# Kernel tuning notes

Hardware: AMD Instinct MI355X
Metric: run time of the kernel (lower is better)

Reference implementation:

```python
import jax, jax.numpy as jnp
import numpy as np

DIM_H = 384
EPS = 0.5
HID = 768
NN = 3   # num_normal_labels (B,I,O)
NL = 7   # num_labels (O, B/I x POS/NEG/NEU)


def _make_w_trans():
    # ote_vocab: B=0, I=1, O=2 ; ts_vocab: O=0, B-POS=1, B-NEG=2, B-NEU=3, I-POS=4, I-NEG=5, I-NEU=6
    W = np.zeros((NN, NL), dtype=np.float32)
    W[0, 1] = W[0, 2] = W[0, 3] = 1.0 / 3.0  # B -> B-*
    W[1, 4] = W[1, 5] = W[1, 6] = 1.0 / 3.0  # I -> I-*
    W[2, 0] = 1.0                            # O -> O
    return jnp.asarray(W)


def setup_inputs() -> dict:
    key = jax.random.key(0)
    ks = jax.random.split(key, 16)
    B, S = 32, 512
    s = 0.02
    inp = {
        'x': jax.random.normal(ks[0], (B, S, HID), jnp.float32),
        'attention_mask': jnp.ones((B, S), jnp.int32),
        'labels': jax.random.randint(ks[1], (B, S), 0, NL, jnp.int32),
        'labels_normal': jax.random.randint(ks[2], (B, S), 0, NN, jnp.int32),
        'W_fc_normal': jax.random.normal(ks[3], (HID, NN), jnp.float32) * s,
        'b_fc_normal': jnp.zeros((NN,), jnp.float32),
        'w_ih_f': jax.random.normal(ks[4], (4 * DIM_H, HID), jnp.float32) * s,
        'w_hh_f': jax.random.normal(ks[5], (4 * DIM_H, DIM_H), jnp.float32) * s,
        'b_f': jnp.zeros((4 * DIM_H,), jnp.float32),
        'w_ih_b': jax.random.normal(ks[6], (4 * DIM_H, HID), jnp.float32) * s,
        'w_hh_b': jax.random.normal(ks[7], (4 * DIM_H, DIM_H), jnp.float32) * s,
        'b_b': jnp.zeros((4 * DIM_H,), jnp.float32),
        'W_gate': jax.random.uniform(ks[8], (2 * DIM_H, 2 * DIM_H), jnp.float32, -0.2, 0.2),
        'W_fc_upper': jax.random.normal(ks[9], (2 * DIM_H, NL), jnp.float32) * s,
        'b_fc_upper': jnp.zeros((NL,), jnp.float32),
        'W_trans': _make_w_trans(),
    }
    return inp


def _lstm_dir(xs, w_ih, w_hh, b):
    # xs: [S, B, HID] time-major; PyTorch gate order i,f,g,o
    B = xs.shape[1]
    pre = jnp.einsum('sbh,gh->sbg', xs, w_ih) + b  # precompute input projections

    def step(carry, p_t):
        h, c = carry
        g = p_t + h @ w_hh.T
        i, f, gg, o = jnp.split(g, 4, axis=-1)
        c = jax.nn.sigmoid(f) * c + jax.nn.sigmoid(i) * jnp.tanh(gg)
        h = jax.nn.sigmoid(o) * jnp.tanh(c)
        return (h, c), h

    init = (jnp.zeros((B, DIM_H), xs.dtype), jnp.zeros((B, DIM_H), xs.dtype))
    _, hs = jax.lax.scan(step, init, pre)
    return hs  # [S, B, DIM_H]


def _masked_ce(logits, labels, mask):
    logp = jax.nn.log_softmax(logits, axis=-1)
    nll = -jnp.take_along_axis(logp, labels[..., None].astype(jnp.int32), axis=-1)[..., 0]
    m = mask.astype(logits.dtype)
    return jnp.sum(nll * m) / jnp.sum(m)


def reference(x, attention_mask, labels, labels_normal, W_fc_normal, b_fc_normal,
              w_ih_f, w_hh_f, b_f, w_ih_b, w_hh_b, b_b, W_gate,
              W_fc_upper, b_fc_upper, W_trans):
    z_t = x @ W_fc_normal + b_fc_normal                      # [B,S,NN]
    loss = _masked_ce(z_t, labels_normal, attention_mask)

    xs = jnp.transpose(x, (1, 0, 2))                         # [S,B,HID]
    hf = _lstm_dir(xs, w_ih_f, w_hh_f, b_f)
    hb = _lstm_dir(xs[::-1], w_ih_b, w_hh_b, b_b)[::-1]
    h_s = jnp.concatenate([hf, hb], axis=-1)                 # [S,B,2*DIM_H]

    # gated highway recurrence: gates depend only on h_s -> batched matmul + linear scan
    g = jax.nn.sigmoid(h_s @ W_gate)                         # [S,B,768]

    def gate_step(h_prev, inp):
        ht, gt = inp
        h = gt * ht + (1.0 - gt) * h_prev
        return h, h

    _, rest = jax.lax.scan(gate_step, h_s[0], (h_s[1:], g[1:]))
    h_tilde = jnp.concatenate([h_s[:1], rest], axis=0)       # [S,B,768]
    h_tilde = jnp.transpose(h_tilde, (1, 0, 2))              # [B,S,768]; dropout = identity (eval)

    z_s = h_tilde @ W_fc_upper + b_fc_upper                  # [B,S,NL]
    p = jax.nn.softmax(z_t, axis=-1)
    alpha = EPS * jnp.sum(p * p, axis=-1, keepdims=True)     # [B,S,1]
    z_s_prime = z_t @ W_trans                                # [B,S,NL]
    z_s_tilde = z_s_prime * alpha + z_s * (1.0 - alpha)

    loss = loss + _masked_ce(z_s_tilde, labels, attention_mask)
    return loss, z_s_tilde
```

## Files before the change

kernel.cpp:

```cpp
#include <hip/hip_runtime.h>

#define B_SZ   32
#define S_LEN  512
#define HID    768
#define DH     384
#define G4     1536
#define NPOS   16384
#define EPS_C  0.5f
#define NCH    24576
#define CHK    64
#define NCHK   8

typedef _Float16 h2 __attribute__((ext_vector_type(2)));
typedef short bf16x8 __attribute__((ext_vector_type(8)));
typedef float f32x4 __attribute__((ext_vector_type(4)));

static __device__ __forceinline__ float sigm(float x) { return 1.0f / (1.0f + __expf(-x)); }
static __device__ __forceinline__ float tanh_fast(float x) {
    return 1.0f - 2.0f / (__expf(2.0f * x) + 1.0f);
}

static __device__ __forceinline__ unsigned short f2bf(float f) {
    union { float f; unsigned u; } v; v.f = f;
    unsigned r = v.u + 0x7FFF + ((v.u >> 16) & 1);
    return (unsigned short)(r >> 16);
}
static __device__ __forceinline__ float bf2f(unsigned short u) {
    union { unsigned u; float f; } v; v.u = ((unsigned)u) << 16; return v.f;
}

static __device__ __forceinline__ float wred(float v) {
#pragma unroll
    for (int off = 32; off > 0; off >>= 1) v += __shfl_down(v, off, 64);
    return v;
}

static __device__ __forceinline__ float dot2acc(h2 a, h2 b, float c) {
#if __has_builtin(__builtin_amdgcn_fdot2)
    return __builtin_amdgcn_fdot2(a, b, c, false);
#else
    return c + (float)a.x * (float)b.x + (float)a.y * (float)b.y;
#endif
}

__global__ void wprep(const float* __restrict__ wf, const float* __restrict__ wb,
                      unsigned* __restrict__ wpk) {
    int gid = blockIdx.x * 256 + threadIdx.x;
    int d = (gid >= 294912) ? 1 : 0;
    int j = gid - d * 294912;
    const float* src = d ? wb : wf;
    _Float16 a = (_Float16)src[2 * j];
    _Float16 b = (_Float16)src[2 * j + 1];
    unsigned pa = __builtin_bit_cast(unsigned short, a);
    unsigned pb = __builtin_bit_cast(unsigned short, b);
    wpk[(size_t)d * 294912 + j] = pa | (pb << 16);
}

__global__ __launch_bounds__(256) void cast_bf16(
    const float* __restrict__ src, unsigned short* __restrict__ dst, int n4) {
    int i = blockIdx.x * 256 + threadIdx.x;
    if (i >= n4) return;
    float4 v = *(const float4*)(src + (size_t)i * 4);
    ushort4 o;
    o.x = f2bf(v.x); o.y = f2bf(v.y); o.z = f2bf(v.z); o.w = f2bf(v.w);
    *(ushort4*)(dst + (size_t)i * 4) = o;
}

__global__ __launch_bounds__(256) void wgt_prep(
    const float* __restrict__ Wg, unsigned short* __restrict__ Wgt) {
    int i = blockIdx.x * 256 + threadIdx.x;
    int k = i / 768, n = i - k * 768;
    Wgt[(size_t)n * 768 + k] = f2bf(Wg[i]);
}

__global__ __launch_bounds__(256) void zt_kernel(
    const float* __restrict__ x, const int* __restrict__ amask,
    const int* __restrict__ labn, const float* __restrict__ Wfc,
    const float* __restrict__ bfc, const float* __restrict__ Wtr,
    float* __restrict__ alpha, float* __restrict__ zsp,
    float* __restrict__ p0, float* __restrict__ p2) {
    const int gid  = blockIdx.x * blockDim.x + threadIdx.x;
    const int pos  = gid >> 6, lane = gid & 63, wv = threadIdx.x >> 6;
    __shared__ float r0[4], r2[4];
    const float* xp = x + (size_t)pos * HID;
    float a0 = 0.f, a1 = 0.f, a2 = 0.f;
#pragma unroll
    for (int j = 0; j < 12; ++j) {
        int k = lane + (j << 6);
        float xv = xp[k];
        a0 += xv * Wfc[k * 3 + 0];
        a1 += xv * Wfc[k * 3 + 1];
        a2 += xv * Wfc[k * 3 + 2];
    }
    a0 = wred(a0); a1 = wred(a1); a2 = wred(a2);
    if (lane == 0) {
        float z0 = a0 + bfc[0], z1 = a1 + bfc[1], z2 = a2 + bfc[2];
        float mx = fmaxf(z0, fmaxf(z1, z2));
        float e0 = __expf(z0 - mx), e1 = __expf(z1 - mx), e2 = __expf(z2 - mx);
        float se = e0 + e1 + e2;
        float m  = (float)amask[pos];
        int  lab = labn[pos];
        float zl = (lab == 0) ? z0 : ((lab == 1) ? z1 : z2);
        r0[wv] = (mx + __logf(se) - zl) * m;
        r2[wv] = m;
        float q0 = e0 / se, q1 = e1 / se, q2 = e2 / se;
        alpha[pos] = EPS_C * (q0 * q0 + q1 * q1 + q2 * q2);
#pragma unroll
        for (int cc = 0; cc < 7; ++cc)
            zsp[(size_t)pos * 7 + cc] = z0 * Wtr[cc] + z1 * Wtr[7 + cc] + z2 * Wtr[14 + cc];
    }
    __syncthreads();
    if (threadIdx.x == 0) {
        p0[blockIdx.x] = r0[0] + r0[1] + r0[2] + r0[3];
        p2[blockIdx.x] = r2[0] + r2[1] + r2[2] + r2[3];
    }
}

__global__ __launch_bounds__(256) void gemm_mfma(
    const unsigned short* __restrict__ A, const unsigned short* __restrict__ B,
    const float* __restrict__ bias, void* __restrict__ Cout,
    int M, int N, int K, int mode) {
    __shared__ __align__(16) unsigned short As[128][40];
    __shared__ __align__(16) unsigned short Bs[128][40];
    const int tid = threadIdx.x;
    const int m0 = blockIdx.y * 128, n0 = blockIdx.x * 128;
    const int wave = tid >> 6, lane = tid & 63;
    const int wm = (wave & 1) * 64, wn = (wave >> 1) * 64;
    const int lm = lane & 15, quad = lane >> 4;
    f32x4 acc[4][4] = {};

    for (int k0 = 0; k0 < K; k0 += 32) {
#pragma unroll
        for (int r = 0; r < 2; ++r) {
            int seg = tid + r * 256;
            int row = seg >> 2, c16 = (seg & 3) << 3;
            uint4 va = *(const uint4*)(A + (size_t)(m0 + row) * K + k0 + c16);
            *(uint4*)&As[row][c16] = va;
            uint4 vb = *(const uint4*)(B + (size_t)(n0 + row) * K + k0 + c16);
            *(uint4*)&Bs[row][c16] = vb;
        }
        __syncthreads();
        bf16x8 af[4], bfr[4];
#pragma unroll
        for (int i = 0; i < 4; ++i) {
            af[i]  = *(const bf16x8*)&As[wm + i * 16 + lm][quad * 8];
            bfr[i] = *(const bf16x8*)&Bs[wn + i * 16 + lm][quad * 8];
        }
#pragma unroll
        for (int mi = 0; mi < 4; ++mi)
#pragma unroll
            for (int ni = 0; ni < 4; ++ni)
                acc[mi][ni] = __builtin_amdgcn_mfma_f32_16x16x32_bf16(
                    af[mi], bfr[ni], acc[mi][ni], 0, 0, 0);
        __syncthreads();
    }

    const int rbase = quad * 4;
#pragma unroll
    for (int mi = 0; mi < 4; ++mi) {
#pragma unroll
        for (int ni = 0; ni < 4; ++ni) {
            const int col = n0 + wn + ni * 16 + lm;
            const float bv = (mode == 0) ? bias[col] : 0.0f;
#pragma unroll
            for (int r = 0; r < 4; ++r) {
                const int row = m0 + wm + mi * 16 + rbase + r;
                float v = acc[mi][ni][r];
                if (mode == 0)
                    ((unsigned short*)Cout)[(size_t)row * N + col] = f2bf(v + bv);
                else
                    ((unsigned short*)Cout)[(size_t)row * N + col] = f2bf(sigm(v));
            }
        }
    }
}

#define WLOAD(i) const uint4 wr##i = wq[i];
#define WDOT(i) \
    a0 = dot2acc(__builtin_bit_cast(h2, wr##i.x), hp[4*(i)+0], a0); \
    a1 = dot2acc(__builtin_bit_cast(h2, wr##i.y), hp[4*(i)+1], a1); \
    a2 = dot2acc(__builtin_bit_cast(h2, wr##i.z), hp[4*(i)+2], a2); \
    a3 = dot2acc(__builtin_bit_cast(h2, wr##i.w), hp[4*(i)+3], a3);

__global__ __launch_bounds__(768) void lstm_scan5(
    const unsigned* __restrict__ wpk,
    const unsigned short* __restrict__ pre,
    unsigned short* __restrict__ h_sb,
    unsigned long long* __restrict__ hx64) {
    const int blk   = blockIdx.x;
    const int chain = blk & 63;
    const int bp    = blk >> 6;
    const int d = chain >> 5, b = chain & 31;
    const int tid = threadIdx.x;
    const int r = tid >> 1, p = tid & 1;
    const int g = r / 96;
    const int u = r - g * 96;
    const int base = bp * 96;
    const int G = g * 384 + base + u;

    __shared__ __align__(16) _Float16 lh16[2][384];
    __shared__ float    lpreV[384];
    __shared__ unsigned lpreT[384];

    const uint4* wq = (const uint4*)(wpk + ((size_t)d * 1536 + G) * 192 + p * 96);
    WLOAD(0)  WLOAD(1)  WLOAD(2)  WLOAD(3)  WLOAD(4)  WLOAD(5)
    WLOAD(6)  WLOAD(7)  WLOAD(8)  WLOAD(9)  WLOAD(10) WLOAD(11)
    WLOAD(12) WLOAD(13) WLOAD(14) WLOAD(15) WLOAD(16) WLOAD(17)
    WLOAD(18) WLOAD(19) WLOAD(20) WLOAD(21) WLOAD(22) WLOAD(23)

    const unsigned short* prb = pre + ((size_t)d * B_SZ + b) * S_LEN * G4;
    float c = 0.0f;

    for (int s = 0; s < S_LEN; ++s) {
        const int t = d ? (S_LEN - 1 - s) : s;
        const int lb = s & 1;
        float prev = bf2f(prb[(size_t)t * G4 + G]);

        if (s == 0) {
            if (tid < 384) { lh16[0][tid] = (_Float16)0.0f; lpreT[tid] = 0xFFFFFFFFu; }
        } else if (tid < 288) {
            const int uu = tid + (tid >= base ? 96 : 0);
            const unsigned long long* srcp =
                hx64 + ((size_t)((s - 1) & 1) * 64 + chain) * 384 + uu;
            unsigned long long v =
                __hip_atomic_load(srcp, __ATOMIC_RELAXED, __HIP_MEMORY_SCOPE_AGENT);
            while ((unsigned)(v >> 32) != (unsigned)(s - 1)) {
                __builtin_amdgcn_s_sleep(1);
                v = __hip_atomic_load(srcp, __ATOMIC_RELAXED, __HIP_MEMORY_SCOPE_AGENT);
            }
            lh16[lb][uu] = (_Float16)__builtin_bit_cast(float, (unsigned)v);
        }
        __syncthreads();

        {
            const h2* hp = ((const h2*)lh16[lb]) + p * 96;
            float a0 = (p == 0) ? prev : 0.0f, a1 = 0.f, a2 = 0.f, a3 = 0.f;
            WDOT(0)  WDOT(1)  WDOT(2)  WDOT(3)  WDOT(4)  WDOT(5)
            WDOT(6)  WDOT(7)  WDOT(8)  WDOT(9)  WDOT(10) WDOT(11)
            WDOT(12) WDOT(13) WDOT(14) WDOT(15) WDOT(16) WDOT(17)
            WDOT(18) WDOT(19) WDOT(20) WDOT(21) WDOT(22) WDOT(23)
            float acc = (a0 + a1) + (a2 + a3);
            float full = acc + __shfl_xor(acc, 1, 64);
            if (p == 0) {
                lpreV[r] = full;
                __hip_atomic_store(&lpreT[r], (unsigned)s, __ATOMIC_RELEASE,
                                   __HIP_MEMORY_SCOPE_WORKGROUP);
            }
        }

        if (tid < 96) {
            const unsigned sv = (unsigned)s;
#pragma unroll
            for (int j = 0; j < 4; ++j) {
                unsigned* tp = &lpreT[j * 96 + tid];
                while (__hip_atomic_load(tp, __ATOMIC_ACQUIRE,
                                         __HIP_MEMORY_SCOPE_WORKGROUP) != sv) {}
            }
            float gi = lpreV[tid], gf = lpreV[96 + tid];
            float gg = lpreV[192 + tid], go = lpreV[288 + tid];
            c = sigm(gf) * c + sigm(gi) * tanh_fast(gg);
            float h = sigm(go) * tanh_fast(c);
            unsigned long long v = ((unsigned long long)sv << 32)
                                 | (unsigned long long)__builtin_bit_cast(unsigned, h);
            __hip_atomic_store(hx64 + ((size_t)lb * 64 + chain) * 384 + base + tid,
                               v, __ATOMIC_RELAXED, __HIP_MEMORY_SCOPE_AGENT);
            h_sb[((size_t)t * B_SZ + b) * HID + d * DH + base + tid] = f2bf(h);
            lh16[lb ^ 1][base + tid] = (_Float16)h;
        }
    }
}

__global__ __launch_bounds__(256) void gscanA(
    const unsigned short* __restrict__ g, const unsigned short* __restrict__ hsb,
    float2* __restrict__ ab) {
    int id = blockIdx.x * 256 + threadIdx.x;
    int chunk = id / NCH, chain = id - chunk * NCH;
    int t0 = chunk * CHK;
    float A = 1.f, Bv = 0.f;
    for (int i = 0; i < CHK; ++i) {
        int t = t0 + i;
        size_t idx = (size_t)t * NCH + chain;
        float gv = bf2f(g[idx]);
        float hv = bf2f(hsb[idx]);
        float a = (t == 0) ? 0.f : (1.f - gv);
        float bb = (t == 0) ? hv : gv * hv;
        A  = a * A;
        Bv = a * Bv + bb;
    }
    ab[id] = make_float2(A, Bv);
}

__global__ __launch_bounds__(256) void gscanB(
    const float2* __restrict__ ab, float* __restrict__ cin) {
    int chain = blockIdx.x * 256 + threadIdx.x;
    float h = 0.f;
#pragma unroll
    for (int j = 0; j < NCHK; ++j) {
        cin[(size_t)j * NCH + chain] = h;
        float2 t = ab[(size_t)j * NCH + chain];
        h = t.x * h + t.y;
    }
}

__global__ __launch_bounds__(256) void gscanC(
    const unsigned short* __restrict__ g, unsigned short* __restrict__ hsb,
    const float* __restrict__ cin) {
    int id = blockIdx.x * 256 + threadIdx.x;
    int chunk = id / NCH, chain = id - chunk * NCH;
    int t0 = chunk * CHK;
    float h = cin[(size_t)chunk * NCH + chain];
    for (int i = 0; i < CHK; ++i) {
        int t = t0 + i;
        size_t idx = (size_t)t * NCH + chain;
        float gv = bf2f(g[idx]);
        float v  = bf2f(hsb[idx]);
        h = (t == 0) ? v : (gv * v + (1.f - gv) * h);
        hsb[idx] = f2bf(h);
    }
}

__global__ __launch_bounds__(256) void final_k(
    const unsigned short* __restrict__ ht, const float* __restrict__ Wup,
    const float* __restrict__ bup, const float* __restrict__ alpha,
    const float* __restrict__ zsp, const int* __restrict__ labels,
    const int* __restrict__ amask, float* __restrict__ out, float* __restrict__ p1) {
    const int gid = blockIdx.x * blockDim.x + threadIdx.x;
    const int pos = gid >> 6, lane = gid & 63, wv = threadIdx.x >> 6;
    __shared__ float r1[4];
    const int bb = pos >> 9, tt = pos & 511;
    const unsigned short* hp = ht + (size_t)tt * (B_SZ * HID) + (size_t)bb * HID;
    float acc[7] = {};
#pragma unroll
    for (int j = 0; j < 12; ++j) {
        int k = lane + (j << 6);
        float hv = bf2f(hp[k]);
        const float* wr = Wup + k * 7;
#pragma unroll
        for (int cc = 0; cc < 7; ++cc) acc[cc] += hv * wr[cc];
    }
#pragma unroll
    for (int cc = 0; cc < 7; ++cc) acc[cc] = wred(acc[cc]);
    if (lane == 0) {
        float al = alpha[pos];
        float z[7], mx = -1e30f;
#pragma unroll
        for (int cc = 0; cc < 7; ++cc) {
            float v = acc[cc] + bup[cc];
            v = zsp[(size_t)pos * 7 + cc] * al + v * (1.0f - al);
            z[cc] = v;
            mx = fmaxf(mx, v);
            out[1 + (size_t)pos * 7 + cc] = v;
        }
        float se = 0.f;
#pragma unroll
        for (int cc = 0; cc < 7; ++cc) se += __expf(z[cc] - mx);
        float lse = mx + __logf(se);
        int lab = labels[pos];
        float zl = z[0];
#pragma unroll
        for (int cc = 1; cc < 7; ++cc) if (lab == cc) zl = z[cc];
        float m = (float)amask[pos];
        r1[wv] = (lse - zl) * m;
    }
    __syncthreads();
    if (threadIdx.x == 0)
        p1[blockIdx.x] = r1[0] + r1[1] + r1[2] + r1[3];
}

__global__ __launch_bounds__(256) void loss_k(
    const float* __restrict__ p0, const float* __restrict__ p1,
    const float* __restrict__ p2, float* __restrict__ out) {
    const int tid = threadIdx.x, lane = tid & 63, wv = tid >> 6;
    __shared__ float rs[4][3];
    float s0 = 0.f, s1 = 0.f, s2 = 0.f;
    for (int i = tid; i < 4096; i += 256) {
        s0 += p0[i]; s1 += p1[i]; s2 += p2[i];
    }
    s0 = wred(s0); s1 = wred(s1); s2 = wred(s2);
    if (lane == 0) { rs[wv][0] = s0; rs[wv][1] = s1; rs[wv][2] = s2; }
    __syncthreads();
    if (tid == 0) {
        float t0 = rs[0][0] + rs[1][0] + rs[2][0] + rs[3][0];
        float t1 = rs[0][1] + rs[1][1] + rs[2][1] + rs[3][1];
        float t2 = rs[0][2] + rs[1][2] + rs[2][2] + rs[3][2];
        out[0] = t0 / t2 + t1 / t2;
    }
}

extern "C" void kernel_launch(void* const* d_in, const int* in_sizes, int n_in,
                              void* d_out, int out_size, void* d_ws, size_t ws_size,
                              hipStream_t stream) {
    const float* x     = (const float*)d_in[0];
    const int*   amask = (const int*)d_in[1];
    const int*   labels= (const int*)d_in[2];
    const int*   labn  = (const int*)d_in[3];
    const float* Wfc   = (const float*)d_in[4];
    const float* bfc   = (const float*)d_in[5];
    const float* wihf  = (const float*)d_in[6];
    const float* whhf  = (const float*)d_in[7];
    const float* bf    = (const float*)d_in[8];
    const float* wihb  = (const float*)d_in[9];
    const float* whhb  = (const float*)d_in[10];
    const float* bb    = (const float*)d_in[11];
    const float* Wg    = (const float*)d_in[12];
    const float* Wup   = (const float*)d_in[13];
    const float* bup   = (const float*)d_in[14];
    const float* Wtr   = (const float*)d_in[15];
    float* out = (float*)d_out;
    (void)in_sizes; (void)n_in; (void)out_size; (void)ws_size;

    char* ws = (char*)d_ws;
    size_t off = 0;
    auto alloc = [&](size_t bytes) -> char* {
        char* p = ws + off;
        off = (off + bytes + 255) & ~(size_t)255;
        return p;
    };
    unsigned* w16buf    = (unsigned*)alloc((size_t)2 * 1536 * 192 * 4);
    unsigned short* pre = (unsigned short*)alloc((size_t)2 * NPOS * G4 * 2);
    unsigned short* xb  = (unsigned short*)alloc((size_t)NPOS * HID * 2);
    unsigned short* wfb = (unsigned short*)alloc((size_t)G4 * HID * 2);
    unsigned short* wbb = (unsigned short*)alloc((size_t)G4 * HID * 2);
    unsigned short* wgt = (unsigned short*)alloc((size_t)HID * HID * 2);
    float* alpha        = (float*)alloc((size_t)NPOS * 4);
    float* zsp          = (float*)alloc((size_t)NPOS * 7 * 4);
    unsigned long long* hx64 = (unsigned long long*)alloc((size_t)2 * 64 * 384 * 8);
    float2* ab          = (float2*)alloc((size_t)NCHK * NCH * 8);
    float* cin          = (float*)alloc((size_t)NCHK * NCH * 4);
    float* part0        = (float*)alloc(4096 * 4);
    float* part1        = (float*)alloc(4096 * 4);
    float* part2        = (float*)alloc(4096 * 4);
    unsigned short* gbuf = (unsigned short*)pre;
    unsigned short* h_sb = xb;


    wprep<<<2304, 256, 0, stream>>>(whhf, whhb, w16buf);
    cast_bf16<<<12288, 256, 0, stream>>>(x, xb, NPOS * HID / 4);
    cast_bf16<<<1152, 256, 0, stream>>>(wihf, wfb, G4 * HID / 4);
    cast_bf16<<<1152, 256, 0, stream>>>(wihb, wbb, G4 * HID / 4);
    wgt_prep<<<2304, 256, 0, stream>>>(Wg, wgt);

    zt_kernel<<<4096, 256, 0, stream>>>(x, amask, labn, Wfc, bfc, Wtr, alpha, zsp,
                                        part0, part2);

    gemm_mfma<<<dim3(12, 128), 256, 0, stream>>>(xb, wfb, bf, pre, NPOS, G4, HID, 0);
    gemm_mfma<<<dim3(12, 128), 256, 0, stream>>>(xb, wbb, bb, pre + (size_t)NPOS * G4,
                                                 NPOS, G4, HID, 0);

    lstm_scan5<<<256, 768, 0, stream>>>(w16buf, pre, h_sb, hx64);

    gemm_mfma<<<dim3(6, 128), 256, 0, stream>>>(h_sb, wgt, nullptr, gbuf, NPOS, HID, HID, 1);

    gscanA<<<768, 256, 0, stream>>>(gbuf, h_sb, ab);
    gscanB<<<96, 256, 0, stream>>>(ab, cin);
    gscanC<<<768, 256, 0, stream>>>(gbuf, h_sb, cin);

    final_k<<<4096, 256, 0, stream>>>(h_sb, Wup, bup, alpha, zsp, labels, amask, out, part1);

    loss_k<<<1, 256, 0, stream>>>(part0, part1, part2, out);
}
```

Before: 1.270 ms.

## Repartition LSTM scan so each block handles four chains over a row slice

```diff
diff --git a/kernel.cpp b/kernel.cpp
--- a/kernel.cpp
+++ b/kernel.cpp
@@ -175,97 +175,138 @@
     }
 }
 
-#define WLOAD(i) const uint4 wr##i = wq[i];
-#define WDOT(i) \
-    a0 = dot2acc(__builtin_bit_cast(h2, wr##i.x), hp[4*(i)+0], a0); \
-    a1 = dot2acc(__builtin_bit_cast(h2, wr##i.y), hp[4*(i)+1], a1); \
-    a2 = dot2acc(__builtin_bit_cast(h2, wr##i.z), hp[4*(i)+2], a2); \
-    a3 = dot2acc(__builtin_bit_cast(h2, wr##i.w), hp[4*(i)+3], a3);
-
-__global__ __launch_bounds__(768) void lstm_scan5(
+#define D16(W, X, A, Bx) { const uint4 xx = (X); \
+    A  = dot2acc(__builtin_bit_cast(h2, W.x), __builtin_bit_cast(h2, xx.x), A); \
+    Bx = dot2acc(__builtin_bit_cast(h2, W.y), __builtin_bit_cast(h2, xx.y), Bx); \
+    A  = dot2acc(__builtin_bit_cast(h2, W.z), __builtin_bit_cast(h2, xx.z), A); \
+    Bx = dot2acc(__builtin_bit_cast(h2, W.w), __builtin_bit_cast(h2, xx.w), Bx); }
+
+__global__ __launch_bounds__(768)
+__attribute__((amdgpu_waves_per_eu(3, 3)))
+void lstm_scan6(
     const unsigned* __restrict__ wpk,
     const unsigned short* __restrict__ pre,
     unsigned short* __restrict__ h_sb,
     unsigned long long* __restrict__ hx64) {
-    const int blk   = blockIdx.x;
-    const int chain = blk & 63;
-    const int bp    = blk >> 6;
-    const int d = chain >> 5, b = chain & 31;
+    const int blk = blockIdx.x;
+    const int grp = blk & 15;
+    const int rp  = blk >> 4;
+    const int d   = grp >> 3;
     const int tid = threadIdx.x;
-    const int r = tid >> 1, p = tid & 1;
-    const int g = r / 96;
-    const int u = r - g * 96;
-    const int base = bp * 96;
-    const int G = g * 384 + base + u;
-
-    __shared__ __align__(16) _Float16 lh16[2][384];
+    const int r   = tid >> 3;
+    const int p   = tid & 7;
+    const int g   = r / 24;
+    const int u   = r - g * 24;
+    const int G   = g * 384 + rp * 24 + u;
+
+    __shared__ __align__(16) _Float16 lh16[2][4][384];
     __shared__ float    lpreV[384];
     __shared__ unsigned lpreT[384];
 
-    const uint4* wq = (const uint4*)(wpk + ((size_t)d * 1536 + G) * 192 + p * 96);
-    WLOAD(0)  WLOAD(1)  WLOAD(2)  WLOAD(3)  WLOAD(4)  WLOAD(5)
-    WLOAD(6)  WLOAD(7)  WLOAD(8)  WLOAD(9)  WLOAD(10) WLOAD(11)
-    WLOAD(12) WLOAD(13) WLOAD(14) WLOAD(15) WLOAD(16) WLOAD(17)
-    WLOAD(18) WLOAD(19) WLOAD(20) WLOAD(21) WLOAD(22) WLOAD(23)
-
-    const unsigned short* prb = pre + ((size_t)d * B_SZ + b) * S_LEN * G4;
+    const uint4* wq = (const uint4*)wpk + (size_t)(d * 1536 + G) * 48 + p * 6;
+    const uint4 w0 = wq[0], w1 = wq[1], w2 = wq[2],
+                w3 = wq[3], w4 = wq[4], w5 = wq[5];
+
+    const int chp = grp * 4 + (p & 3);
+    const unsigned short* prb =
+        pre + ((size_t)d * B_SZ + (chp & 31)) * S_LEN * G4 + G;
+
     float c = 0.0f;
 
     for (int s = 0; s < S_LEN; ++s) {
-        const int t = d ? (S_LEN - 1 - s) : s;
+        const int t  = d ? (S_LEN - 1 - s) : s;
         const int lb = s & 1;
-        float prev = bf2f(prb[(size_t)t * G4 + G]);
+        float prev = 0.0f;
+        if (p < 4) prev = bf2f(prb[(size_t)t * G4]);
 
         if (s == 0) {
-            if (tid < 384) { lh16[0][tid] = (_Float16)0.0f; lpreT[tid] = 0xFFFFFFFFu; }
-        } else if (tid < 288) {
-            const int uu = tid + (tid >= base ? 96 : 0);
-            const unsigned long long* srcp =
-                hx64 + ((size_t)((s - 1) & 1) * 64 + chain) * 384 + uu;
-            unsigned long long v =
-                __hip_atomic_load(srcp, __ATOMIC_RELAXED, __HIP_MEMORY_SCOPE_AGENT);
-            while ((unsigned)(v >> 32) != (unsigned)(s - 1)) {
-                __builtin_amdgcn_s_sleep(1);
-                v = __hip_atomic_load(srcp, __ATOMIC_RELAXED, __HIP_MEMORY_SCOPE_AGENT);
+            if (tid < 384) lpreT[tid] = 0xFFFFFFFFu;
+            const int cia = (tid >= 384) ? 1 : 0;
+            const int j = tid - cia * 384;
+            lh16[0][cia][j]     = (_Float16)0.0f;
+            lh16[0][cia + 2][j] = (_Float16)0.0f;
+        } else {
+            const int cia = (tid >= 384) ? 1 : 0;
+            const int j = tid - cia * 384;
+            if ((unsigned)(j - rp * 24) >= 24u) {
+                const unsigned long long* sp0 =
+                    hx64 + ((size_t)((s - 1) & 1) * 64 + grp * 4 + cia) * 384 + j;
+                const unsigned want = (unsigned)(s - 1);
+                unsigned long long v0 =
+                    __hip_atomic_load(sp0, __ATOMIC_RELAXED, __HIP_MEMORY_SCOPE_AGENT);
+                unsigned long long v1 =
+                    __hip_atomic_load(sp0 + 768, __ATOMIC_RELAXED, __HIP_MEMORY_SCOPE_AGENT);
+                while ((unsigned)(v0 >> 32) != want) {
+                    __builtin_amdgcn_s_sleep(1);
+                    v0 = __hip_atomic_load(sp0, __ATOMIC_RELAXED, __HIP_MEMORY_SCOPE_AGENT);
+                }
+                while ((unsigned)(v1 >> 32) != want) {
+                    __builtin_amdgcn_s_sleep(1);
+                    v1 = __hip_atomic_load(sp0 + 768, __ATOMIC_RELAXED, __HIP_MEMORY_SCOPE_AGENT);
+                }
+                lh16[lb][cia][j]     = (_Float16)__builtin_bit_cast(float, (unsigned)v0);
+                lh16[lb][cia + 2][j] = (_Float16)__builtin_bit_cast(float, (unsigned)v1);
             }
-            lh16[lb][uu] = (_Float16)__builtin_bit_cast(float, (unsigned)v);
         }
         __syncthreads();
 
         {
-            const h2* hp = ((const h2*)lh16[lb]) + p * 96;
-            float a0 = (p == 0) ? prev : 0.0f, a1 = 0.f, a2 = 0.f, a3 = 0.f;
-            WDOT(0)  WDOT(1)  WDOT(2)  WDOT(3)  WDOT(4)  WDOT(5)
-            WDOT(6)  WDOT(7)  WDOT(8)  WDOT(9)  WDOT(10) WDOT(11)
-            WDOT(12) WDOT(13) WDOT(14) WDOT(15) WDOT(16) WDOT(17)
-            WDOT(18) WDOT(19) WDOT(20) WDOT(21) WDOT(22) WDOT(23)
-            float acc = (a0 + a1) + (a2 + a3);
-            float full = acc + __shfl_xor(acc, 1, 64);
-            if (p == 0) {
-                lpreV[r] = full;
-                __hip_atomic_store(&lpreT[r], (unsigned)s, __ATOMIC_RELEASE,
+            const char* hb = (const char*)&lh16[lb][0][0] + p * 96;
+            const uint4* h0 = (const uint4*)(hb);
+            const uint4* h1 = (const uint4*)(hb + 768);
+            const uint4* h2q = (const uint4*)(hb + 1536);
+            const uint4* h3 = (const uint4*)(hb + 2304);
+            float a0 = 0.f, a1 = 0.f, a2 = 0.f, a3 = 0.f;
+            float b0 = 0.f, b1 = 0.f, b2 = 0.f, b3 = 0.f;
+            if      (p == 0) a0 = prev;
+            else if (p == 1) a1 = prev;
+            else if (p == 2) a2 = prev;
+            else if (p == 3) a3 = prev;
+            D16(w0, h0[0], a0, b0) D16(w1, h0[1], a0, b0) D16(w2, h0[2], a0, b0)
+            D16(w3, h0[3], a0, b0) D16(w4, h0[4], a0, b0) D16(w5, h0[5], a0, b0)
+            D16(w0, h1[0], a1, b1) D16(w1, h1[1], a1, b1) D16(w2, h1[2], a1, b1)
+            D16(w3, h1[3], a1, b1) D16(w4, h1[4], a1, b1) D16(w5, h1[5], a1, b1)
+            D16(w0, h2q[0], a2, b2) D16(w1, h2q[1], a2, b2) D16(w2, h2q[2], a2, b2)
+            D16(w3, h2q[3], a2, b2) D16(w4, h2q[4], a2, b2) D16(w5, h2q[5], a2, b2)
+            D16(w0, h3[0], a3, b3) D16(w1, h3[1], a3, b3) D16(w2, h3[2], a3, b3)
+            D16(w3, h3[3], a3, b3) D16(w4, h3[4], a3, b3) D16(w5, h3[5], a3, b3)
+            a0 += b0; a1 += b1; a2 += b2; a3 += b3;
+#pragma unroll
+            for (int off = 1; off < 8; off <<= 1) {
+                a0 += __shfl_xor(a0, off, 64);
+                a1 += __shfl_xor(a1, off, 64);
+                a2 += __shfl_xor(a2, off, 64);
+                a3 += __shfl_xor(a3, off, 64);
+            }
+            if (p < 4) {
+                float av = (p == 0) ? a0 : (p == 1) ? a1 : (p == 2) ? a2 : a3;
+                lpreV[p * 96 + r] = av;
+                __hip_atomic_store(&lpreT[p * 96 + r], (unsigned)s, __ATOMIC_RELEASE,
                                    __HIP_MEMORY_SCOPE_WORKGROUP);
             }
         }
 
         if (tid < 96) {
+            const int ci = tid / 24, uu = tid - ci * 24;
             const unsigned sv = (unsigned)s;
-#pragma unroll
-            for (int j = 0; j < 4; ++j) {
-                unsigned* tp = &lpreT[j * 96 + tid];
-                while (__hip_atomic_load(tp, __ATOMIC_ACQUIRE,
+            unsigned* tp = &lpreT[ci * 96 + uu];
+#pragma unroll
+            for (int jj = 0; jj < 4; ++jj) {
+                while (__hip_atomic_load(tp + jj * 24, __ATOMIC_ACQUIRE,
                                          __HIP_MEMORY_SCOPE_WORKGROUP) != sv) {}
             }
-            float gi = lpreV[tid], gf = lpreV[96 + tid];
-            float gg = lpreV[192 + tid], go = lpreV[288 + tid];
+            float gi = lpreV[ci * 96 + uu],      gf = lpreV[ci * 96 + 24 + uu];
+            float gg = lpreV[ci * 96 + 48 + uu], go = lpreV[ci * 96 + 72 + uu];
             c = sigm(gf) * c + sigm(gi) * tanh_fast(gg);
             float h = sigm(go) * tanh_fast(c);
+            const int chain = grp * 4 + ci, bb2 = chain & 31;
+            const int rowg = rp * 24 + uu;
             unsigned long long v = ((unsigned long long)sv << 32)
                                  | (unsigned long long)__builtin_bit_cast(unsigned, h);
-            __hip_atomic_store(hx64 + ((size_t)lb * 64 + chain) * 384 + base + tid,
+            __hip_atomic_store(hx64 + ((size_t)lb * 64 + chain) * 384 + rowg,
                                v, __ATOMIC_RELAXED, __HIP_MEMORY_SCOPE_AGENT);
-            h_sb[((size_t)t * B_SZ + b) * HID + d * DH + base + tid] = f2bf(h);
-            lh16[lb ^ 1][base + tid] = (_Float16)h;
+            h_sb[((size_t)t * B_SZ + bb2) * HID + d * DH + rowg] = f2bf(h);
+            lh16[lb ^ 1][ci][rowg] = (_Float16)h;
         }
     }
 }
@@ -447,7 +488,7 @@
     gemm_mfma<<<dim3(12, 128), 256, 0, stream>>>(xb, wbb, bb, pre + (size_t)NPOS * G4,
                                                  NPOS, G4, HID, 0);
 
-    lstm_scan5<<<256, 768, 0, stream>>>(w16buf, pre, h_sb, hx64);
+    lstm_scan6<<<256, 768, 0, stream>>>(w16buf, pre, h_sb, hx64);
 
     gemm_mfma<<<dim3(6, 128), 256, 0, stream>>>(h_sb, wgt, nullptr, gbuf, NPOS, HID, HID, 1);
 
```

Measured after the change: 2.028 ms. 59.7% more time.

## Process two LSTM chains per block with 8-way K split and halved weight registers

Applied to the files above, without the earlier changes.

```diff
diff --git a/kernel.cpp b/kernel.cpp
--- a/kernel.cpp
+++ b/kernel.cpp
@@ -42,6 +42,8 @@
     return c + (float)a.x * (float)b.x + (float)a.y * (float)b.y;
 #endif
 }
+
+static __device__ __forceinline__ h2 hcast(unsigned u) { return __builtin_bit_cast(h2, u); }
 
 __global__ void wprep(const float* __restrict__ wf, const float* __restrict__ wb,
                       unsigned* __restrict__ wpk) {
@@ -175,97 +177,140 @@
     }
 }
 
-#define WLOAD(i) const uint4 wr##i = wq[i];
-#define WDOT(i) \
-    a0 = dot2acc(__builtin_bit_cast(h2, wr##i.x), hp[4*(i)+0], a0); \
-    a1 = dot2acc(__builtin_bit_cast(h2, wr##i.y), hp[4*(i)+1], a1); \
-    a2 = dot2acc(__builtin_bit_cast(h2, wr##i.z), hp[4*(i)+2], a2); \
-    a3 = dot2acc(__builtin_bit_cast(h2, wr##i.w), hp[4*(i)+3], a3);
-
-__global__ __launch_bounds__(768) void lstm_scan5(
+#define DD(WA, WB, X, SA0, SB0, SA1, SB1) { const uint4 xx = (X); \
+    SA0 = dot2acc(hcast(WA.x), hcast(xx.x), SA0); \
+    SB0 = dot2acc(hcast(WA.y), hcast(xx.y), SB0); \
+    SA0 = dot2acc(hcast(WA.z), hcast(xx.z), SA0); \
+    SB0 = dot2acc(hcast(WA.w), hcast(xx.w), SB0); \
+    SA1 = dot2acc(hcast(WB.x), hcast(xx.x), SA1); \
+    SB1 = dot2acc(hcast(WB.y), hcast(xx.y), SB1); \
+    SA1 = dot2acc(hcast(WB.z), hcast(xx.z), SA1); \
+    SB1 = dot2acc(hcast(WB.w), hcast(xx.w), SB1); }
+
+__global__ __launch_bounds__(768)
+__attribute__((amdgpu_waves_per_eu(3, 3)))
+void lstm_scan7(
     const unsigned* __restrict__ wpk,
     const unsigned short* __restrict__ pre,
     unsigned short* __restrict__ h_sb,
     unsigned long long* __restrict__ hx64) {
-    const int blk   = blockIdx.x;
-    const int chain = blk & 63;
-    const int bp    = blk >> 6;
-    const int d = chain >> 5, b = chain & 31;
+    const int blk = blockIdx.x;
+    const int q   = blk & 31;
+    const int rp  = blk >> 5;
+    const int d   = q >> 4;
     const int tid = threadIdx.x;
-    const int r = tid >> 1, p = tid & 1;
-    const int g = r / 96;
-    const int u = r - g * 96;
-    const int base = bp * 96;
-    const int G = g * 384 + base + u;
-
-    __shared__ __align__(16) _Float16 lh16[2][384];
+    const int r2  = tid >> 3;
+    const int p   = tid & 7;
+    const int g   = r2 / 24;
+    const int up  = r2 - g * 24;
+    const int G0  = g * 384 + rp * 48 + up * 2;
+
+    __shared__ __align__(16) _Float16 lh16[2][2][384];
     __shared__ float    lpreV[384];
     __shared__ unsigned lpreT[384];
 
-    const uint4* wq = (const uint4*)(wpk + ((size_t)d * 1536 + G) * 192 + p * 96);
-    WLOAD(0)  WLOAD(1)  WLOAD(2)  WLOAD(3)  WLOAD(4)  WLOAD(5)
-    WLOAD(6)  WLOAD(7)  WLOAD(8)  WLOAD(9)  WLOAD(10) WLOAD(11)
-    WLOAD(12) WLOAD(13) WLOAD(14) WLOAD(15) WLOAD(16) WLOAD(17)
-    WLOAD(18) WLOAD(19) WLOAD(20) WLOAD(21) WLOAD(22) WLOAD(23)
-
-    const unsigned short* prb = pre + ((size_t)d * B_SZ + b) * S_LEN * G4;
+    const uint4* wqa = (const uint4*)wpk + (size_t)(d * 1536 + G0) * 48 + p * 6;
+    const uint4* wqb = wqa + 48;
+    const uint4 wa0 = wqa[0], wa1 = wqa[1], wa2 = wqa[2],
+                wa3 = wqa[3], wa4 = wqa[4], wa5 = wqa[5];
+    const uint4 wb0 = wqb[0], wb1 = wqb[1], wb2 = wqb[2],
+                wb3 = wqb[3], wb4 = wqb[4], wb5 = wqb[5];
+
+    const int cip = p >> 1, rsel = p & 1;
+    const unsigned short* prb =
+        pre + ((size_t)d * B_SZ + ((q * 2 + cip) & 31)) * S_LEN * G4 + G0 + rsel;
+
+    const int sci = (tid >= 384) ? 1 : 0;
+    const int sj  = tid - sci * 384;
+    const int sch = q * 2 + sci;
+    const bool sown = ((unsigned)(sj - rp * 48) < 48u);
+
     float c = 0.0f;
 
     for (int s = 0; s < S_LEN; ++s) {
-        const int t = d ? (S_LEN - 1 - s) : s;
+        const int t  = d ? (S_LEN - 1 - s) : s;
         const int lb = s & 1;
-        float prev = bf2f(prb[(size_t)t * G4 + G]);
+        float prev = 0.0f;
+        if (p < 4) prev = bf2f(prb[(size_t)t * G4]);
 
         if (s == 0) {
-            if (tid < 384) { lh16[0][tid] = (_Float16)0.0f; lpreT[tid] = 0xFFFFFFFFu; }
-        } else if (tid < 288) {
-            const int uu = tid + (tid >= base ? 96 : 0);
-            const unsigned long long* srcp =
-                hx64 + ((size_t)((s - 1) & 1) * 64 + chain) * 384 + uu;
+            if (tid < 384) lpreT[tid] = 0xFFFFFFFFu;
+            lh16[0][sci][sj] = (_Float16)0.0f;
+        } else if (!sown) {
+            const unsigned long long* sp =
+                hx64 + ((size_t)((s - 1) & 1) * 64 + sch) * 384 + sj;
+            const unsigned want = (unsigned)(s - 1);
             unsigned long long v =
-                __hip_atomic_load(srcp, __ATOMIC_RELAXED, __HIP_MEMORY_SCOPE_AGENT);
-            while ((unsigned)(v >> 32) != (unsigned)(s - 1)) {
+                __hip_atomic_load(sp, __ATOMIC_RELAXED, __HIP_MEMORY_SCOPE_AGENT);
+            while ((unsigned)(v >> 32) != want) {
                 __builtin_amdgcn_s_sleep(1);
-                v = __hip_atomic_load(srcp, __ATOMIC_RELAXED, __HIP_MEMORY_SCOPE_AGENT);
+                v = __hip_atomic_load(sp, __ATOMIC_RELAXED, __HIP_MEMORY_SCOPE_AGENT);
             }
-            lh16[lb][uu] = (_Float16)__builtin_bit_cast(float, (unsigned)v);
+            lh16[lb][sci][sj] = (_Float16)__builtin_bit_cast(float, (unsigned)v);
         }
         __syncthreads();
 
         {
-            const h2* hp = ((const h2*)lh16[lb]) + p * 96;
-            float a0 = (p == 0) ? prev : 0.0f, a1 = 0.f, a2 = 0.f, a3 = 0.f;
-            WDOT(0)  WDOT(1)  WDOT(2)  WDOT(3)  WDOT(4)  WDOT(5)
-            WDOT(6)  WDOT(7)  WDOT(8)  WDOT(9)  WDOT(10) WDOT(11)
-            WDOT(12) WDOT(13) WDOT(14) WDOT(15) WDOT(16) WDOT(17)
-            WDOT(18) WDOT(19) WDOT(20) WDOT(21) WDOT(22) WDOT(23)
-            float acc = (a0 + a1) + (a2 + a3);
-            float full = acc + __shfl_xor(acc, 1, 64);
-            if (p == 0) {
-                lpreV[r] = full;
-                __hip_atomic_store(&lpreT[r], (unsigned)s, __ATOMIC_RELEASE,
+            const uint4* h0 = (const uint4*)&lh16[lb][0][0] + p * 6;
+            const uint4* h1 = (const uint4*)&lh16[lb][1][0] + p * 6;
+            float s00a = 0.f, s00b = 0.f, s01a = 0.f, s01b = 0.f;
+            float s10a = 0.f, s10b = 0.f, s11a = 0.f, s11b = 0.f;
+            if      (p == 0) s00a = prev;
+            else if (p == 1) s01a = prev;
+            else if (p == 2) s10a = prev;
+            else if (p == 3) s11a = prev;
+            DD(wa0, wb0, h0[0], s00a, s00b, s01a, s01b)
+            DD(wa1, wb1, h0[1], s00a, s00b, s01a, s01b)
+            DD(wa2, wb2, h0[2], s00a, s00b, s01a, s01b)
+            DD(wa3, wb3, h0[3], s00a, s00b, s01a, s01b)
+            DD(wa4, wb4, h0[4], s00a, s00b, s01a, s01b)
+            DD(wa5, wb5, h0[5], s00a, s00b, s01a, s01b)
+            DD(wa0, wb0, h1[0], s10a, s10b, s11a, s11b)
+            DD(wa1, wb1, h1[1], s10a, s10b, s11a, s11b)
+            DD(wa2, wb2, h1[2], s10a, s10b, s11a, s11b)
+            DD(wa3, wb3, h1[3], s10a, s10b, s11a, s11b)
+            DD(wa4, wb4, h1[4], s10a, s10b, s11a, s11b)
+            DD(wa5, wb5, h1[5], s10a, s10b, s11a, s11b)
+            float r00 = s00a + s00b, r01 = s01a + s01b;
+            float r10 = s10a + s10b, r11 = s11a + s11b;
+#pragma unroll
+            for (int off = 1; off < 8; off <<= 1) {
+                r00 += __shfl_xor(r00, off, 64);
+                r01 += __shfl_xor(r01, off, 64);
+                r10 += __shfl_xor(r10, off, 64);
+                r11 += __shfl_xor(r11, off, 64);
+            }
+            if (p < 4) {
+                float rv = (p == 0) ? r00 : (p == 1) ? r01 : (p == 2) ? r10 : r11;
+                const int li = cip * 192 + g * 48 + up * 2 + rsel;
+                lpreV[li] = rv;
+                __hip_atomic_store(&lpreT[li], (unsigned)s, __ATOMIC_RELEASE,
                                    __HIP_MEMORY_SCOPE_WORKGROUP);
             }
         }
 
         if (tid < 96) {
+            const int ci = tid >> 6 ? 1 : (tid >= 48);
+            const int urow = tid - ci * 48;
+            const int lbase = ci * 192 + urow;
             const unsigned sv = (unsigned)s;
 #pragma unroll
-            for (int j = 0; j < 4; ++j) {
-                unsigned* tp = &lpreT[j * 96 + tid];
-                while (__hip_atomic_load(tp, __ATOMIC_ACQUIRE,
+            for (int jj = 0; jj < 4; ++jj) {
+                while (__hip_atomic_load(&lpreT[lbase + jj * 48], __ATOMIC_ACQUIRE,
                                          __HIP_MEMORY_SCOPE_WORKGROUP) != sv) {}
             }
-            float gi = lpreV[tid], gf = lpreV[96 + tid];
-            float gg = lpreV[192 + tid], go = lpreV[288 + tid];
+            float gi = lpreV[lbase],      gf = lpreV[lbase + 48];
+            float gg = lpreV[lbase + 96], go = lpreV[lbase + 144];
             c = sigm(gf) * c + sigm(gi) * tanh_fast(gg);
             float h = sigm(go) * tanh_fast(c);
+            const int chain = q * 2 + ci, bb2 = chain & 31;
+            const int j = rp * 48 + urow;
             unsigned long long v = ((unsigned long long)sv << 32)
                                  | (unsigned long long)__builtin_bit_cast(unsigned, h);
-            __hip_atomic_store(hx64 + ((size_t)lb * 64 + chain) * 384 + base + tid,
+            __hip_atomic_store(hx64 + ((size_t)lb * 64 + chain) * 384 + j,
                                v, __ATOMIC_RELAXED, __HIP_MEMORY_SCOPE_AGENT);
-            h_sb[((size_t)t * B_SZ + b) * HID + d * DH + base + tid] = f2bf(h);
-            lh16[lb ^ 1][base + tid] = (_Float16)h;
+            h_sb[((size_t)t * B_SZ + bb2) * HID + d * DH + j] = f2bf(h);
+            lh16[lb ^ 1][ci][j] = (_Float16)h;
         }
     }
 }
@@ -447,7 +492,7 @@
     gemm_mfma<<<dim3(12, 128), 256, 0, stream>>>(xb, wbb, bb, pre + (size_t)NPOS * G4,
                                                  NPOS, G4, HID, 0);
 
-    lstm_scan5<<<256, 768, 0, stream>>>(w16buf, pre, h_sb, hx64);
+    lstm_scan7<<<256, 768, 0, stream>>>(w16buf, pre, h_sb, hx64);
 
     gemm_mfma<<<dim3(6, 128), 256, 0, stream>>>(h_sb, wgt, nullptr, gbuf, NPOS, HID, HID, 1);
 
```

After: 1.631 ms. 28.4% more time.

## Restructure LSTM scan to 4-lane split with half weights reloaded each step

Applied to the files above, without the earlier changes.

```diff
diff --git a/kernel.cpp b/kernel.cpp
--- a/kernel.cpp
+++ b/kernel.cpp
@@ -40,6 +40,18 @@
     return __builtin_amdgcn_fdot2(a, b, c, false);
 #else
     return c + (float)a.x * (float)b.x + (float)a.y * (float)b.y;
+#endif
+}
+
+static __device__ __forceinline__ h2 hcast(unsigned u) { return __builtin_bit_cast(h2, u); }
+
+template <int CTRL>
+static __device__ __forceinline__ float qperm_add(float v) {
+#if __has_builtin(__builtin_amdgcn_mov_dpp)
+    int o = __builtin_amdgcn_mov_dpp(__builtin_bit_cast(int, v), CTRL, 0xF, 0xF, true);
+    return v + __builtin_bit_cast(float, o);
+#else
+    return v + __shfl_xor(v, (CTRL == 0xB1) ? 1 : 2, 64);
 #endif
 }
 
@@ -175,46 +187,53 @@
     }
 }
 
-#define WLOAD(i) const uint4 wr##i = wq[i];
-#define WDOT(i) \
-    a0 = dot2acc(__builtin_bit_cast(h2, wr##i.x), hp[4*(i)+0], a0); \
-    a1 = dot2acc(__builtin_bit_cast(h2, wr##i.y), hp[4*(i)+1], a1); \
-    a2 = dot2acc(__builtin_bit_cast(h2, wr##i.z), hp[4*(i)+2], a2); \
-    a3 = dot2acc(__builtin_bit_cast(h2, wr##i.w), hp[4*(i)+3], a3);
-
-__global__ __launch_bounds__(768) void lstm_scan5(
+#define DOT8(W, H, A0, A1) { \
+    A0 = dot2acc(hcast(W.x), hcast(H.x), A0); \
+    A1 = dot2acc(hcast(W.y), hcast(H.y), A1); \
+    A0 = dot2acc(hcast(W.z), hcast(H.z), A0); \
+    A1 = dot2acc(hcast(W.w), hcast(H.w), A1); }
+
+__global__ __launch_bounds__(768)
+__attribute__((amdgpu_waves_per_eu(3, 3)))
+void lstm_scan8(
     const unsigned* __restrict__ wpk,
     const unsigned short* __restrict__ pre,
     unsigned short* __restrict__ h_sb,
     unsigned long long* __restrict__ hx64) {
     const int blk   = blockIdx.x;
     const int chain = blk & 63;
-    const int bp    = blk >> 6;
+    const int rp    = blk >> 6;
     const int d = chain >> 5, b = chain & 31;
     const int tid = threadIdx.x;
-    const int r = tid >> 1, p = tid & 1;
-    const int g = r / 96;
-    const int u = r - g * 96;
-    const int base = bp * 96;
-    const int G = g * 384 + base + u;
+    const int j = tid >> 2;
+    const int p = tid & 3;
+    const int ga = j / 96, ua = j - ga * 96;
+    const int base = rp * 96;
+    const int Ga = ga * 384 + base + ua;
 
     __shared__ __align__(16) _Float16 lh16[2][384];
     __shared__ float    lpreV[384];
     __shared__ unsigned lpreT[384];
 
-    const uint4* wq = (const uint4*)(wpk + ((size_t)d * 1536 + G) * 192 + p * 96);
-    WLOAD(0)  WLOAD(1)  WLOAD(2)  WLOAD(3)  WLOAD(4)  WLOAD(5)
-    WLOAD(6)  WLOAD(7)  WLOAD(8)  WLOAD(9)  WLOAD(10) WLOAD(11)
-    WLOAD(12) WLOAD(13) WLOAD(14) WLOAD(15) WLOAD(16) WLOAD(17)
-    WLOAD(18) WLOAD(19) WLOAD(20) WLOAD(21) WLOAD(22) WLOAD(23)
-
-    const unsigned short* prb = pre + ((size_t)d * B_SZ + b) * S_LEN * G4;
+    const uint4* wqA = (const uint4*)wpk + ((size_t)d * 1536 + Ga) * 48 + p * 12;
+    const uint4* wqB = wqA + 36864;
+    const uint4 wa0 = wqA[0], wa1 = wqA[1], wa2  = wqA[2],  wa3  = wqA[3],
+                wa4 = wqA[4], wa5 = wqA[5], wa6  = wqA[6],  wa7  = wqA[7],
+                wa8 = wqA[8], wa9 = wqA[9], wa10 = wqA[10], wa11 = wqA[11];
+
+    const unsigned short* prb =
+        pre + ((size_t)d * B_SZ + b) * S_LEN * G4 + Ga + ((p == 1) ? 768 : 0);
+
     float c = 0.0f;
 
     for (int s = 0; s < S_LEN; ++s) {
-        const int t = d ? (S_LEN - 1 - s) : s;
+        const int t  = d ? (S_LEN - 1 - s) : s;
         const int lb = s & 1;
-        float prev = bf2f(prb[(size_t)t * G4 + G]);
+        float prev = 0.0f;
+        if (p < 2) prev = bf2f(prb[(size_t)t * G4]);
+        const uint4 xb0 = wqB[0], xb1 = wqB[1], xb2  = wqB[2],  xb3  = wqB[3],
+                    xb4 = wqB[4], xb5 = wqB[5], xb6  = wqB[6],  xb7  = wqB[7],
+                    xb8 = wqB[8], xb9 = wqB[9], xb10 = wqB[10], xb11 = wqB[11];
 
         if (s == 0) {
             if (tid < 384) { lh16[0][tid] = (_Float16)0.0f; lpreT[tid] = 0xFFFFFFFFu; }
@@ -233,17 +252,29 @@
         __syncthreads();
 
         {
-            const h2* hp = ((const h2*)lh16[lb]) + p * 96;
-            float a0 = (p == 0) ? prev : 0.0f, a1 = 0.f, a2 = 0.f, a3 = 0.f;
-            WDOT(0)  WDOT(1)  WDOT(2)  WDOT(3)  WDOT(4)  WDOT(5)
-            WDOT(6)  WDOT(7)  WDOT(8)  WDOT(9)  WDOT(10) WDOT(11)
-            WDOT(12) WDOT(13) WDOT(14) WDOT(15) WDOT(16) WDOT(17)
-            WDOT(18) WDOT(19) WDOT(20) WDOT(21) WDOT(22) WDOT(23)
-            float acc = (a0 + a1) + (a2 + a3);
-            float full = acc + __shfl_xor(acc, 1, 64);
+            const uint4* hq = (const uint4*)&lh16[lb][0] + p * 12;
+            const uint4 hv0 = hq[0], hv1 = hq[1], hv2  = hq[2],  hv3  = hq[3],
+                        hv4 = hq[4], hv5 = hq[5], hv6  = hq[6],  hv7  = hq[7],
+                        hv8 = hq[8], hv9 = hq[9], hv10 = hq[10], hv11 = hq[11];
+            float a0 = 0.f, a1 = 0.f, b0 = 0.f, b1 = 0.f;
+            DOT8(wa0, hv0, a0, a1)  DOT8(wa1, hv1, a0, a1)  DOT8(wa2,  hv2,  a0, a1)
+            DOT8(wa3, hv3, a0, a1)  DOT8(wa4, hv4, a0, a1)  DOT8(wa5,  hv5,  a0, a1)
+            DOT8(wa6, hv6, a0, a1)  DOT8(wa7, hv7, a0, a1)  DOT8(wa8,  hv8,  a0, a1)
+            DOT8(wa9, hv9, a0, a1)  DOT8(wa10, hv10, a0, a1) DOT8(wa11, hv11, a0, a1)
+            DOT8(xb0, hv0, b0, b1)  DOT8(xb1, hv1, b0, b1)  DOT8(xb2,  hv2,  b0, b1)
+            DOT8(xb3, hv3, b0, b1)  DOT8(xb4, hv4, b0, b1)  DOT8(xb5,  hv5,  b0, b1)
+            DOT8(xb6, hv6, b0, b1)  DOT8(xb7, hv7, b0, b1)  DOT8(xb8,  hv8,  b0, b1)
+            DOT8(xb9, hv9, b0, b1)  DOT8(xb10, hv10, b0, b1) DOT8(xb11, hv11, b0, b1)
+            float sa = a0 + a1, sb = b0 + b1;
+            sa = qperm_add<0xB1>(sa); sa = qperm_add<0x4E>(sa);
+            sb = qperm_add<0xB1>(sb); sb = qperm_add<0x4E>(sb);
             if (p == 0) {
-                lpreV[r] = full;
-                __hip_atomic_store(&lpreT[r], (unsigned)s, __ATOMIC_RELEASE,
+                lpreV[j] = sa + prev;
+                __hip_atomic_store(&lpreT[j], (unsigned)s, __ATOMIC_RELEASE,
+                                   __HIP_MEMORY_SCOPE_WORKGROUP);
+            } else if (p == 1) {
+                lpreV[j + 192] = sb + prev;
+                __hip_atomic_store(&lpreT[j + 192], (unsigned)s, __ATOMIC_RELEASE,
                                    __HIP_MEMORY_SCOPE_WORKGROUP);
             }
         }
@@ -251,8 +282,8 @@
         if (tid < 96) {
             const unsigned sv = (unsigned)s;
 #pragma unroll
-            for (int j = 0; j < 4; ++j) {
-                unsigned* tp = &lpreT[j * 96 + tid];
+            for (int jj = 0; jj < 4; ++jj) {
+                unsigned* tp = &lpreT[jj * 96 + tid];
                 while (__hip_atomic_load(tp, __ATOMIC_ACQUIRE,
                                          __HIP_MEMORY_SCOPE_WORKGROUP) != sv) {}
             }
@@ -447,7 +478,7 @@
     gemm_mfma<<<dim3(12, 128), 256, 0, stream>>>(xb, wbb, bb, pre + (size_t)NPOS * G4,
                                                  NPOS, G4, HID, 0);
 
-    lstm_scan5<<<256, 768, 0, stream>>>(w16buf, pre, h_sb, hx64);
+    lstm_scan8<<<256, 768, 0, stream>>>(w16buf, pre, h_sb, hx64);
 
     gemm_mfma<<<dim3(6, 128), 256, 0, stream>>>(h_sb, wgt, nullptr, gbuf, NPOS, HID, HID, 1);
 
```

After: 1.371 ms. +7.9%, slower.
